# Performance work log

Measured on AMD Instinct MI355X. Metric: run time of the kernel, lower is better.

Reference implementation:

```python
import jax, jax.numpy as jnp
import numpy as np

ALPHA = 100.0
EPS = 1e-12  # matches torch F.normalize eps


def l2norm(v, axis):
    n = jnp.linalg.norm(v, axis=axis, keepdims=True)
    return v / jnp.maximum(n, EPS)


def setup_inputs() -> dict:
    key = jax.random.key(0)
    k1, k2 = jax.random.split(key)
    x = jax.random.normal(k1, (32, 512, 32, 32), dtype=jnp.float32)
    vocabs = jax.random.uniform(k2, (64, 512), dtype=jnp.float32)  # torch.rand init
    return {"x": x, "vocabs": vocabs}


def reference(x, vocabs):
    # x: [N, C, H, W]; vocabs: [K, C]
    N, C, H, W = x.shape
    K = vocabs.shape[0]
    x = l2norm(x, axis=1)                       # normalize descriptors over C
    xf = x.reshape(N, C, H * W)                 # [N, C, P]

    # 1x1 conv with weight = 2*alpha*vocabs, bias = -alpha*||vocabs||
    w = 2.0 * ALPHA * vocabs                    # [K, C]
    b = -ALPHA * jnp.linalg.norm(vocabs, axis=1)  # [K]
    logits = jnp.einsum('ncp,kc->nkp', xf, w) + b[None, :, None]
    a = jax.nn.softmax(logits, axis=1)          # soft assignment over K

    # Distributive rewrite of sum_p a[n,k,p]*(x[n,c,p] - vocabs[k,c])
    vlad = jnp.einsum('nkp,ncp->nkc', a, xf) - a.sum(-1)[:, :, None] * vocabs[None]
    vlad = l2norm(vlad, axis=2)                 # intra-normalization
    vlad = vlad.reshape(N, K * C)
    return l2norm(vlad, axis=1)
```

## Files before the change

kernel.cpp:

```cpp
#include <hip/hip_runtime.h>
#include <math.h>
#include <stdint.h>

#define ALPHA 100.0f
#define EPSN 1e-12f

typedef __attribute__((ext_vector_type(8))) short bf16x8;
typedef __attribute__((ext_vector_type(16))) float f32x16;
typedef __attribute__((ext_vector_type(4))) float f32x4;
typedef __attribute__((ext_vector_type(4))) unsigned int u32x4;

static __device__ __forceinline__ uint32_t f2bf(float f) {
    uint32_t u = __builtin_bit_cast(uint32_t, f);
    return (u + 0x7FFFu + ((u >> 16) & 1u)) >> 16;
}
static __device__ __forceinline__ float bfhi(uint32_t u) {
    return __builtin_bit_cast(float, u & 0xFFFF0000u);
}
static __device__ __forceinline__ uint32_t packbf(float a, float b) {
    return f2bf(a) | (f2bf(b) << 16);
}
static __device__ __forceinline__ void lds_barrier() {
    asm volatile("s_waitcnt lgkmcnt(0)\n\ts_barrier" ::: "memory");
}

__global__ __launch_bounds__(64) void prep_kernel(const float* __restrict__ v,
                                                  unsigned short* __restrict__ vh,
                                                  unsigned short* __restrict__ vl,
                                                  float* __restrict__ bias,
                                                  float* __restrict__ az) {
    int k = blockIdx.x, lane = threadIdx.x;
    az[k * 64 + lane] = 0.f;
    const float* row = v + k * 512;
    float ssq = 0.f;
#pragma unroll
    for (int i = 0; i < 8; ++i) {
        int c = lane + 64 * i;
        float f = row[c];
        ssq = fmaf(f, f, ssq);
        uint32_t hi = f2bf(f);
        uint32_t lo = f2bf(f - __builtin_bit_cast(float, hi << 16));
        vh[k * 512 + c] = (unsigned short)hi;
        vl[k * 512 + c] = (unsigned short)lo;
    }
#pragma unroll
    for (int off = 32; off > 0; off >>= 1) ssq += __shfl_xor(ssq, off, 64);
    if (lane == 0) bias[k] = -ALPHA * sqrtf(ssq);
}

__global__ __launch_bounds__(512) void fused_kernel(
    const float* __restrict__ x, const unsigned short* __restrict__ vh,
    const unsigned short* __restrict__ vl, const float* __restrict__ bias,
    float* __restrict__ pw, float* __restrict__ asum) {
    __shared__ uint32_t xsh[2][16 * 132];
    __shared__ uint32_t xsl[2][16 * 132];
    __shared__ float ssq_s[16][132];
    __shared__ float ssq_l[128];
    __shared__ float bias_l[64];
    __shared__ float xchm[4][2][32];
    __shared__ float xchs[4][2][32];
    __shared__ float a2f[64 * 132];
    __shared__ uint32_t xv[128 * 68];

    int tid = threadIdx.x, bx = blockIdx.x;
    int n = bx >> 3, pt = bx & 7, pblk = pt << 7;
    int l = tid & 63, w = tid >> 6;
    int kh = w & 1, ps = w >> 1;
    int h = l >> 5, cl = l & 31;
    int r = tid >> 5, q = tid & 31;

    if (tid < 64) bias_l[tid] = bias[tid];

    const float* xg = x + (size_t)n * 524288 + (size_t)(2 * r) * 1024 + pblk + 4 * q;
    const unsigned short* vhg = vh + (size_t)(32 * kh + cl) * 512 + 8 * h;
    const unsigned short* vlg = vl + (size_t)(32 * kh + cl) * 512 + 8 * h;

    f32x16 accA, accB;
#pragma unroll
    for (int i = 0; i < 16; ++i) { accA[i] = 0.f; accB[i] = 0.f; }
    f32x4 ssqv;
#pragma unroll
    for (int i = 0; i < 4; ++i) ssqv[i] = 0.f;

    float4 xa[3], xb[3];
    u32x4 vfh[3][2], vfl[3][2];

#define A_LOAD(slot, cc)                                                       \
    do {                                                                       \
        xa[slot] = *(const float4*)(xg + (size_t)(cc)*32768);                  \
        xb[slot] = *(const float4*)(xg + (size_t)(cc)*32768 + 1024);           \
        vfh[slot][0] = *(const u32x4*)(vhg + (cc)*32);                         \
        vfh[slot][1] = *(const u32x4*)(vhg + (cc)*32 + 16);                    \
        vfl[slot][0] = *(const u32x4*)(vlg + (cc)*32);                         \
        vfl[slot][1] = *(const u32x4*)(vlg + (cc)*32 + 16);                    \
    } while (0)
#define A_STAGE(buf, slot)                                                     \
    do {                                                                       \
        float fa[4] = {xa[slot].x, xa[slot].y, xa[slot].z, xa[slot].w};        \
        float fb[4] = {xb[slot].x, xb[slot].y, xb[slot].z, xb[slot].w};        \
        u32x4 hp, lp;                                                          \
        _Pragma("unroll") for (int i = 0; i < 4; ++i) {                        \
            uint32_t h0 = f2bf(fa[i]);                                         \
            uint32_t l0 = f2bf(fa[i] - bfhi(h0 << 16));                        \
            uint32_t h1 = f2bf(fb[i]);                                         \
            uint32_t l1 = f2bf(fb[i] - bfhi(h1 << 16));                        \
            hp[i] = h0 | (h1 << 16);                                           \
            lp[i] = l0 | (l1 << 16);                                           \
            ssqv[i] = fmaf(fa[i], fa[i], fmaf(fb[i], fb[i], ssqv[i]));         \
        }                                                                      \
        *(u32x4*)&xsh[buf][r * 132 + 4 * q] = hp;                              \
        *(u32x4*)&xsl[buf][r * 132 + 4 * q] = lp;                              \
    } while (0)
#define A_COMPUTE(buf, slot)                                                   \
    do {                                                                       \
        _Pragma("unroll") for (int s = 0; s < 2; ++s) {                        \
            int xb_ = (8 * s + 4 * h) * 132 + 32 * ps + cl;                    \
            u32x4 bhp, blp;                                                    \
            _Pragma("unroll") for (int q2 = 0; q2 < 4; ++q2) {                 \
                bhp[q2] = xsh[buf][xb_ + q2 * 132];                            \
                blp[q2] = xsl[buf][xb_ + q2 * 132];                            \
            }                                                                  \
            bf16x8 ah = __builtin_bit_cast(bf16x8, vfh[slot][s]);              \
            bf16x8 al = __builtin_bit_cast(bf16x8, vfl[slot][s]);              \
            bf16x8 xh_ = __builtin_bit_cast(bf16x8, bhp);                      \
            bf16x8 xl_ = __builtin_bit_cast(bf16x8, blp);                      \
            f32x16& accr = s ? accB : accA;                                    \
            accr = __builtin_amdgcn_mfma_f32_32x32x16_bf16(ah, xh_, accr, 0, 0, 0);\
            accr = __builtin_amdgcn_mfma_f32_32x32x16_bf16(ah, xl_, accr, 0, 0, 0);\
            accr = __builtin_amdgcn_mfma_f32_32x32x16_bf16(al, xh_, accr, 0, 0, 0);\
        }                                                                      \
    } while (0)

    A_LOAD(0, 0);
    A_LOAD(1, 1);
    A_LOAD(2, 2);
    A_STAGE(0, 0);
    lds_barrier();
#pragma unroll
    for (int cc = 0; cc < 16; ++cc) {
        if (cc < 15) A_STAGE((cc + 1) & 1, (cc + 1) % 3);
        A_COMPUTE(cc & 1, cc % 3);
        if (cc < 13) A_LOAD(cc % 3, cc + 3);
        lds_barrier();
    }
#undef A_LOAD
#undef A_STAGE
#undef A_COMPUTE

    *(f32x4*)&ssq_s[r][4 * q] = ssqv;
    __syncthreads();
    if (tid < 128) {
        float s = 0.f;
#pragma unroll
        for (int rr = 0; rr < 16; ++rr) s += ssq_s[rr][tid];
        ssq_l[tid] = s;
    }
    __syncthreads();
    float ssq = ssq_l[32 * ps + cl];
    float sinv = 1.0f / fmaxf(sqrtf(ssq), EPSN);
    float twoAs = 2.0f * ALPHA * sinv;
    float e[16];
    float m = -INFINITY;
#pragma unroll
    for (int rr = 0; rr < 16; ++rr) {
        int k = (rr & 3) + 8 * (rr >> 2) + 4 * h + 32 * kh;
        float lv = fmaf(twoAs, accA[rr] + accB[rr], bias_l[k]);
        e[rr] = lv;
        m = fmaxf(m, lv);
    }
    m = fmaxf(m, __shfl_xor(m, 32, 64));
    if (l < 32) xchm[ps][kh][l] = m;
    __syncthreads();
    m = fmaxf(m, xchm[ps][1 - kh][cl]);
    float ssum = 0.f;
#pragma unroll
    for (int rr = 0; rr < 16; ++rr) {
        e[rr] = expf(e[rr] - m);
        ssum += e[rr];
    }
    ssum += __shfl_xor(ssum, 32, 64);
    if (l < 32) xchs[ps][kh][l] = ssum;
    __syncthreads();
    ssum += xchs[ps][1 - kh][cl];
    float rs = 1.0f / ssum;
    float a2s = rs * sinv;
#pragma unroll
    for (int rr = 0; rr < 16; ++rr) {
        int k = (rr & 3) + 8 * (rr >> 2) + 4 * h + 32 * kh;
        a2f[k * 132 + 32 * ps + cl] = e[rr] * a2s;
        float red = e[rr] * rs;
#pragma unroll
        for (int off = 1; off <= 16; off <<= 1) red += __shfl_xor(red, off, 64);
        if (cl == 0) atomicAdd(&asum[n * 64 + k], red);
    }
    __syncthreads();

    f32x16 va0, va1, va2, va3;
#pragma unroll
    for (int i = 0; i < 16; ++i) { va0[i] = 0.f; va1[i] = 0.f; va2[i] = 0.f; va3[i] = 0.f; }

    int g = tid >> 2, u = tid & 3;
#pragma unroll
    for (int r2 = 0; r2 < 4; ++r2) {
        __syncthreads();
        {
            int c = (g >> 5) * 128 + r2 * 32 + (g & 31);
            const float* xs2 = x + (size_t)n * 524288 + (size_t)c * 1024 + pblk + 32 * u;
            float4 f0 = *(const float4*)(xs2);
            float4 f1 = *(const float4*)(xs2 + 4);
            float4 f2 = *(const float4*)(xs2 + 8);
            float4 f3 = *(const float4*)(xs2 + 12);
            float4 f4 = *(const float4*)(xs2 + 16);
            float4 f5 = *(const float4*)(xs2 + 20);
            float4 f6 = *(const float4*)(xs2 + 24);
            float4 f7 = *(const float4*)(xs2 + 28);
            u32x4 w0, w1, w2, w3;
            w0[0] = packbf(f0.x, f0.y); w0[1] = packbf(f0.z, f0.w);
            w0[2] = packbf(f1.x, f1.y); w0[3] = packbf(f1.z, f1.w);
            w1[0] = packbf(f2.x, f2.y); w1[1] = packbf(f2.z, f2.w);
            w1[2] = packbf(f3.x, f3.y); w1[3] = packbf(f3.z, f3.w);
            w2[0] = packbf(f4.x, f4.y); w2[1] = packbf(f4.z, f4.w);
            w2[2] = packbf(f5.x, f5.y); w2[3] = packbf(f5.z, f5.w);
            w3[0] = packbf(f6.x, f6.y); w3[1] = packbf(f6.z, f6.w);
            w3[2] = packbf(f7.x, f7.y); w3[3] = packbf(f7.z, f7.w);
            int xb0 = g * 68 + 16 * u;
            *(u32x4*)&xv[xb0] = w0;
            *(u32x4*)&xv[xb0 + 4] = w1;
            *(u32x4*)&xv[xb0 + 8] = w2;
            *(u32x4*)&xv[xb0 + 12] = w3;
        }
        __syncthreads();
        f32x16& vac = (r2 == 0) ? va0 : (r2 == 1) ? va1 : (r2 == 2) ? va2 : va3;
#pragma unroll
        for (int mm = 0; mm < 8; ++mm) {
            int ab = (32 * kh + cl) * 132 + 16 * mm + 8 * h;
            u32x4 af;
#pragma unroll
            for (int j = 0; j < 4; ++j)
                af[j] = packbf(a2f[ab + 2 * j], a2f[ab + 2 * j + 1]);
            int bb = (32 * ps + cl) * 68 + 8 * mm + 4 * h;
            u32x4 bf = *(const u32x4*)&xv[bb];
            vac = __builtin_amdgcn_mfma_f32_32x32x16_bf16(
                __builtin_bit_cast(bf16x8, af), __builtin_bit_cast(bf16x8, bf),
                vac, 0, 0, 0);
        }
    }
    float* pwb = pw + (((size_t)n * 8 + pt) * 64) * 512;
#pragma unroll
    for (int r2 = 0; r2 < 4; ++r2) {
        f32x16& vac = (r2 == 0) ? va0 : (r2 == 1) ? va1 : (r2 == 2) ? va2 : va3;
        int c = 128 * ps + 32 * r2 + cl;
#pragma unroll
        for (int rr = 0; rr < 16; ++rr) {
            int k = (rr & 3) + 8 * (rr >> 2) + 4 * h + 32 * kh;
            pwb[(size_t)k * 512 + c] = vac[rr];
        }
    }
}

__global__ __launch_bounds__(512) void combine_kernel(
    const float* __restrict__ pw, const float* __restrict__ asum,
    const float* __restrict__ vocabs, float* __restrict__ out) {
    __shared__ float lv[32768];
    __shared__ float knorm_l[64];
    __shared__ float sc[64];
    __shared__ float tots;

    int n = blockIdx.x, tid = threadIdx.x;
    int kq = tid >> 7, tc = tid & 127;
    const float* pwn = pw + (size_t)n * 262144;

#pragma unroll
    for (int ki = 0; ki < 16; ++ki) {
        int k = kq * 16 + ki;
        float a = asum[n * 64 + k];
        float4 vv = *(const float4*)(vocabs + (size_t)k * 512 + 4 * tc);
        float4 s = make_float4(0.f, 0.f, 0.f, 0.f);
#pragma unroll
        for (int pt = 0; pt < 8; ++pt) {
            float4 p4 = *(const float4*)(pwn + (size_t)pt * 32768 + (size_t)k * 512 + 4 * tc);
            s.x += p4.x; s.y += p4.y; s.z += p4.z; s.w += p4.w;
        }
        s.x = fmaf(-a, vv.x, s.x);
        s.y = fmaf(-a, vv.y, s.y);
        s.z = fmaf(-a, vv.z, s.z);
        s.w = fmaf(-a, vv.w, s.w);
        *(float4*)&lv[k * 512 + 4 * tc] = s;
    }
    __syncthreads();
    {
        int k2 = tid >> 3, j = tid & 7;
        float t2 = 0.f;
#pragma unroll
        for (int i = 0; i < 16; ++i) {
            float4 v4 = *(const float4*)&lv[k2 * 512 + j * 64 + 4 * i];
            t2 += v4.x * v4.x + v4.y * v4.y + v4.z * v4.z + v4.w * v4.w;
        }
        t2 += __shfl_xor(t2, 1, 64);
        t2 += __shfl_xor(t2, 2, 64);
        t2 += __shfl_xor(t2, 4, 64);
        if (j == 0) knorm_l[k2] = t2;
    }
    __syncthreads();
    if (tid < 64) {
        float nk = sqrtf(knorm_l[tid]);
        float inv = 1.0f / fmaxf(nk, EPSN);
        sc[tid] = inv;
        float t = nk * inv;
        float t2 = t * t;
#pragma unroll
        for (int off = 32; off > 0; off >>= 1) t2 += __shfl_xor(t2, off, 64);
        if (tid == 0) tots = t2;
    }
    __syncthreads();
    float invt = 1.0f / fmaxf(sqrtf(tots), EPSN);
    float* on = out + (size_t)n * 32768;
#pragma unroll
    for (int i = 0; i < 64; ++i) {
        int idx = tid + 512 * i;
        on[idx] = lv[idx] * sc[idx >> 9] * invt;
    }
}

extern "C" void kernel_launch(void* const* d_in, const int* in_sizes, int n_in,
                              void* d_out, int out_size, void* d_ws, size_t ws_size,
                              hipStream_t stream) {
    const float* x = (const float*)d_in[0];
    const float* vocabs = (const float*)d_in[1];
    float* out = (float*)d_out;
    char* ws = (char*)d_ws;
    unsigned short* vh = (unsigned short*)(ws);
    unsigned short* vl = (unsigned short*)(ws + 65536);
    float* bias  = (float*)(ws + 131072);
    float* asum  = (float*)(ws + 131328);
    float* pw    = (float*)(ws + 147712);

    prep_kernel<<<64, 64, 0, stream>>>(vocabs, vh, vl, bias, asum);
    fused_kernel<<<256, 512, 0, stream>>>(x, vh, vl, bias, pw, asum);
    combine_kernel<<<32, 512, 0, stream>>>(pw, asum, vocabs, out);
}
```

Before: 152.8 us.

## Stage full bf16 x tile in LDS once and reuse it for both GEMMs

Halves the pixel tile to 64 per block and doubles the grid to 512 blocks. Each block loads and splits its whole x tile (all 512 channels) into LDS up front, replacing the pipelined channel-chunk staging. The second GEMM (assignments times x) now reads the bf16-high copy of x from LDS instead of reloading x from global memory and repacking it. The first GEMM is split over channel halves across warps, with a cross-warp reduction through LDS. The partial-sum buffer doubles in size, so the combine kernel reads 16 partials per image instead of 8, which adds combine traffic and workspace.

```diff
diff --git a/kernel.cpp b/kernel.cpp
--- a/kernel.cpp
+++ b/kernel.cpp
@@ -16,12 +16,6 @@
 }
 static __device__ __forceinline__ float bfhi(uint32_t u) {
     return __builtin_bit_cast(float, u & 0xFFFF0000u);
-}
-static __device__ __forceinline__ uint32_t packbf(float a, float b) {
-    return f2bf(a) | (f2bf(b) << 16);
-}
-static __device__ __forceinline__ void lds_barrier() {
-    asm volatile("s_waitcnt lgkmcnt(0)\n\ts_barrier" ::: "memory");
 }
 
 __global__ __launch_bounds__(64) void prep_kernel(const float* __restrict__ v,
@@ -52,208 +46,194 @@
     const float* __restrict__ x, const unsigned short* __restrict__ vh,
     const unsigned short* __restrict__ vl, const float* __restrict__ bias,
     float* __restrict__ pw, float* __restrict__ asum) {
-    __shared__ uint32_t xsh[2][16 * 132];
-    __shared__ uint32_t xsl[2][16 * 132];
-    __shared__ float ssq_s[16][132];
-    __shared__ float ssq_l[128];
+    __shared__ uint32_t xallh[256 * 66];
+    __shared__ uint32_t xallo[256 * 64];
+    __shared__ float cmb[2][2][16][64];
+    __shared__ unsigned short a2b[64 * 72];
+    __shared__ float ssq_l[64];
     __shared__ float bias_l[64];
-    __shared__ float xchm[4][2][32];
-    __shared__ float xchs[4][2][32];
-    __shared__ float a2f[64 * 132];
-    __shared__ uint32_t xv[128 * 68];
+    __shared__ float xchm[2][2][32];
+    __shared__ float xchs[2][2][32];
 
     int tid = threadIdx.x, bx = blockIdx.x;
-    int n = bx >> 3, pt = bx & 7, pblk = pt << 7;
+    int n = bx >> 4, pt = bx & 15, pblk = pt << 6;
     int l = tid & 63, w = tid >> 6;
-    int kh = w & 1, ps = w >> 1;
     int h = l >> 5, cl = l & 31;
-    int r = tid >> 5, q = tid & 31;
-
-    if (tid < 64) bias_l[tid] = bias[tid];
-
-    const float* xg = x + (size_t)n * 524288 + (size_t)(2 * r) * 1024 + pblk + 4 * q;
-    const unsigned short* vhg = vh + (size_t)(32 * kh + cl) * 512 + 8 * h;
-    const unsigned short* vlg = vl + (size_t)(32 * kh + cl) * 512 + 8 * h;
+
+    if (tid < 64) {
+        ssq_l[tid] = 0.f;
+        bias_l[tid] = bias[tid];
+    }
+
+    int r0 = tid >> 4, q = tid & 15;
+    const float* xgs = x + (size_t)n * 524288 + (size_t)(2 * r0) * 1024 + pblk + 4 * q;
+    float4 va_[8], vb_[8];
+#pragma unroll
+    for (int i = 0; i < 8; ++i) {
+        va_[i] = *(const float4*)(xgs + (size_t)i * 65536);
+        vb_[i] = *(const float4*)(xgs + (size_t)i * 65536 + 1024);
+    }
+    __syncthreads();
+    f32x4 sq;
+#pragma unroll
+    for (int j = 0; j < 4; ++j) sq[j] = 0.f;
+#pragma unroll
+    for (int i = 0; i < 8; ++i) {
+        int R = r0 + 32 * i;
+        float fa[4] = {va_[i].x, va_[i].y, va_[i].z, va_[i].w};
+        float fb[4] = {vb_[i].x, vb_[i].y, vb_[i].z, vb_[i].w};
+        uint32_t hp[4];
+        u32x4 lp;
+#pragma unroll
+        for (int j = 0; j < 4; ++j) {
+            uint32_t h0 = f2bf(fa[j]);
+            uint32_t l0 = f2bf(fa[j] - bfhi(h0 << 16));
+            uint32_t h1 = f2bf(fb[j]);
+            uint32_t l1 = f2bf(fb[j] - bfhi(h1 << 16));
+            hp[j] = h0 | (h1 << 16);
+            lp[j] = l0 | (l1 << 16);
+            sq[j] = fmaf(fa[j], fa[j], fmaf(fb[j], fb[j], sq[j]));
+        }
+        *(uint2*)&xallh[R * 66 + 4 * q] = make_uint2(hp[0], hp[1]);
+        *(uint2*)&xallh[R * 66 + 4 * q + 2] = make_uint2(hp[2], hp[3]);
+        *(u32x4*)&xallo[R * 64 + 4 * q] = lp;
+    }
+#pragma unroll
+    for (int j = 0; j < 4; ++j) atomicAdd(&ssq_l[4 * q + j], sq[j]);
+    __syncthreads();
+
+    int kh = w & 1, pj = (w >> 1) & 1, ch = w >> 2;
+    const unsigned short* vhg = vh + (size_t)(32 * kh + cl) * 512 + 256 * ch + 8 * h;
+    const unsigned short* vlg = vl + (size_t)(32 * kh + cl) * 512 + 256 * ch + 8 * h;
 
     f32x16 accA, accB;
 #pragma unroll
     for (int i = 0; i < 16; ++i) { accA[i] = 0.f; accB[i] = 0.f; }
-    f32x4 ssqv;
-#pragma unroll
-    for (int i = 0; i < 4; ++i) ssqv[i] = 0.f;
-
-    float4 xa[3], xb[3];
-    u32x4 vfh[3][2], vfl[3][2];
-
-#define A_LOAD(slot, cc)                                                       \
-    do {                                                                       \
-        xa[slot] = *(const float4*)(xg + (size_t)(cc)*32768);                  \
-        xb[slot] = *(const float4*)(xg + (size_t)(cc)*32768 + 1024);           \
-        vfh[slot][0] = *(const u32x4*)(vhg + (cc)*32);                         \
-        vfh[slot][1] = *(const u32x4*)(vhg + (cc)*32 + 16);                    \
-        vfl[slot][0] = *(const u32x4*)(vlg + (cc)*32);                         \
-        vfl[slot][1] = *(const u32x4*)(vlg + (cc)*32 + 16);                    \
-    } while (0)
-#define A_STAGE(buf, slot)                                                     \
-    do {                                                                       \
-        float fa[4] = {xa[slot].x, xa[slot].y, xa[slot].z, xa[slot].w};        \
-        float fb[4] = {xb[slot].x, xb[slot].y, xb[slot].z, xb[slot].w};        \
-        u32x4 hp, lp;                                                          \
-        _Pragma("unroll") for (int i = 0; i < 4; ++i) {                        \
-            uint32_t h0 = f2bf(fa[i]);                                         \
-            uint32_t l0 = f2bf(fa[i] - bfhi(h0 << 16));                        \
-            uint32_t h1 = f2bf(fb[i]);                                         \
-            uint32_t l1 = f2bf(fb[i] - bfhi(h1 << 16));                        \
-            hp[i] = h0 | (h1 << 16);                                           \
-            lp[i] = l0 | (l1 << 16);                                           \
-            ssqv[i] = fmaf(fa[i], fa[i], fmaf(fb[i], fb[i], ssqv[i]));         \
-        }                                                                      \
-        *(u32x4*)&xsh[buf][r * 132 + 4 * q] = hp;                              \
-        *(u32x4*)&xsl[buf][r * 132 + 4 * q] = lp;                              \
-    } while (0)
-#define A_COMPUTE(buf, slot)                                                   \
-    do {                                                                       \
-        _Pragma("unroll") for (int s = 0; s < 2; ++s) {                        \
-            int xb_ = (8 * s + 4 * h) * 132 + 32 * ps + cl;                    \
-            u32x4 bhp, blp;                                                    \
-            _Pragma("unroll") for (int q2 = 0; q2 < 4; ++q2) {                 \
-                bhp[q2] = xsh[buf][xb_ + q2 * 132];                            \
-                blp[q2] = xsl[buf][xb_ + q2 * 132];                            \
-            }                                                                  \
-            bf16x8 ah = __builtin_bit_cast(bf16x8, vfh[slot][s]);              \
-            bf16x8 al = __builtin_bit_cast(bf16x8, vfl[slot][s]);              \
-            bf16x8 xh_ = __builtin_bit_cast(bf16x8, bhp);                      \
-            bf16x8 xl_ = __builtin_bit_cast(bf16x8, blp);                      \
-            f32x16& accr = s ? accB : accA;                                    \
-            accr = __builtin_amdgcn_mfma_f32_32x32x16_bf16(ah, xh_, accr, 0, 0, 0);\
-            accr = __builtin_amdgcn_mfma_f32_32x32x16_bf16(ah, xl_, accr, 0, 0, 0);\
-            accr = __builtin_amdgcn_mfma_f32_32x32x16_bf16(al, xh_, accr, 0, 0, 0);\
-        }                                                                      \
-    } while (0)
-
-    A_LOAD(0, 0);
-    A_LOAD(1, 1);
-    A_LOAD(2, 2);
-    A_STAGE(0, 0);
-    lds_barrier();
-#pragma unroll
-    for (int cc = 0; cc < 16; ++cc) {
-        if (cc < 15) A_STAGE((cc + 1) & 1, (cc + 1) % 3);
-        A_COMPUTE(cc & 1, cc % 3);
-        if (cc < 13) A_LOAD(cc % 3, cc + 3);
-        lds_barrier();
-    }
-#undef A_LOAD
-#undef A_STAGE
-#undef A_COMPUTE
-
-    *(f32x4*)&ssq_s[r][4 * q] = ssqv;
-    __syncthreads();
-    if (tid < 128) {
-        float s = 0.f;
-#pragma unroll
-        for (int rr = 0; rr < 16; ++rr) s += ssq_s[rr][tid];
-        ssq_l[tid] = s;
-    }
-    __syncthreads();
-    float ssq = ssq_l[32 * ps + cl];
-    float sinv = 1.0f / fmaxf(sqrtf(ssq), EPSN);
-    float twoAs = 2.0f * ALPHA * sinv;
-    float e[16];
-    float m = -INFINITY;
-#pragma unroll
-    for (int rr = 0; rr < 16; ++rr) {
-        int k = (rr & 3) + 8 * (rr >> 2) + 4 * h + 32 * kh;
-        float lv = fmaf(twoAs, accA[rr] + accB[rr], bias_l[k]);
-        e[rr] = lv;
-        m = fmaxf(m, lv);
-    }
-    m = fmaxf(m, __shfl_xor(m, 32, 64));
-    if (l < 32) xchm[ps][kh][l] = m;
-    __syncthreads();
-    m = fmaxf(m, xchm[ps][1 - kh][cl]);
-    float ssum = 0.f;
-#pragma unroll
-    for (int rr = 0; rr < 16; ++rr) {
-        e[rr] = expf(e[rr] - m);
-        ssum += e[rr];
-    }
-    ssum += __shfl_xor(ssum, 32, 64);
-    if (l < 32) xchs[ps][kh][l] = ssum;
-    __syncthreads();
-    ssum += xchs[ps][1 - kh][cl];
-    float rs = 1.0f / ssum;
-    float a2s = rs * sinv;
-#pragma unroll
-    for (int rr = 0; rr < 16; ++rr) {
-        int k = (rr & 3) + 8 * (rr >> 2) + 4 * h + 32 * kh;
-        a2f[k * 132 + 32 * ps + cl] = e[rr] * a2s;
-        float red = e[rr] * rs;
-#pragma unroll
-        for (int off = 1; off <= 16; off <<= 1) red += __shfl_xor(red, off, 64);
-        if (cl == 0) atomicAdd(&asum[n * 64 + k], red);
-    }
-    __syncthreads();
-
-    f32x16 va0, va1, va2, va3;
-#pragma unroll
-    for (int i = 0; i < 16; ++i) { va0[i] = 0.f; va1[i] = 0.f; va2[i] = 0.f; va3[i] = 0.f; }
-
-    int g = tid >> 2, u = tid & 3;
-#pragma unroll
-    for (int r2 = 0; r2 < 4; ++r2) {
-        __syncthreads();
-        {
-            int c = (g >> 5) * 128 + r2 * 32 + (g & 31);
-            const float* xs2 = x + (size_t)n * 524288 + (size_t)c * 1024 + pblk + 32 * u;
-            float4 f0 = *(const float4*)(xs2);
-            float4 f1 = *(const float4*)(xs2 + 4);
-            float4 f2 = *(const float4*)(xs2 + 8);
-            float4 f3 = *(const float4*)(xs2 + 12);
-            float4 f4 = *(const float4*)(xs2 + 16);
-            float4 f5 = *(const float4*)(xs2 + 20);
-            float4 f6 = *(const float4*)(xs2 + 24);
-            float4 f7 = *(const float4*)(xs2 + 28);
-            u32x4 w0, w1, w2, w3;
-            w0[0] = packbf(f0.x, f0.y); w0[1] = packbf(f0.z, f0.w);
-            w0[2] = packbf(f1.x, f1.y); w0[3] = packbf(f1.z, f1.w);
-            w1[0] = packbf(f2.x, f2.y); w1[1] = packbf(f2.z, f2.w);
-            w1[2] = packbf(f3.x, f3.y); w1[3] = packbf(f3.z, f3.w);
-            w2[0] = packbf(f4.x, f4.y); w2[1] = packbf(f4.z, f4.w);
-            w2[2] = packbf(f5.x, f5.y); w2[3] = packbf(f5.z, f5.w);
-            w3[0] = packbf(f6.x, f6.y); w3[1] = packbf(f6.z, f6.w);
-            w3[2] = packbf(f7.x, f7.y); w3[3] = packbf(f7.z, f7.w);
-            int xb0 = g * 68 + 16 * u;
-            *(u32x4*)&xv[xb0] = w0;
-            *(u32x4*)&xv[xb0 + 4] = w1;
-            *(u32x4*)&xv[xb0 + 8] = w2;
-            *(u32x4*)&xv[xb0 + 12] = w3;
-        }
-        __syncthreads();
-        f32x16& vac = (r2 == 0) ? va0 : (r2 == 1) ? va1 : (r2 == 2) ? va2 : va3;
-#pragma unroll
-        for (int mm = 0; mm < 8; ++mm) {
-            int ab = (32 * kh + cl) * 132 + 16 * mm + 8 * h;
-            u32x4 af;
-#pragma unroll
-            for (int j = 0; j < 4; ++j)
-                af[j] = packbf(a2f[ab + 2 * j], a2f[ab + 2 * j + 1]);
-            int bb = (32 * ps + cl) * 68 + 8 * mm + 4 * h;
-            u32x4 bf = *(const u32x4*)&xv[bb];
-            vac = __builtin_amdgcn_mfma_f32_32x32x16_bf16(
-                __builtin_bit_cast(bf16x8, af), __builtin_bit_cast(bf16x8, bf),
-                vac, 0, 0, 0);
-        }
-    }
-    float* pwb = pw + (((size_t)n * 8 + pt) * 64) * 512;
-#pragma unroll
-    for (int r2 = 0; r2 < 4; ++r2) {
-        f32x16& vac = (r2 == 0) ? va0 : (r2 == 1) ? va1 : (r2 == 2) ? va2 : va3;
-        int c = 128 * ps + 32 * r2 + cl;
+
+    u32x4 pvh[2][2], pvl[2][2];
+    pvh[0][0] = *(const u32x4*)(vhg);
+    pvh[0][1] = *(const u32x4*)(vhg + 16);
+    pvl[0][0] = *(const u32x4*)(vlg);
+    pvl[0][1] = *(const u32x4*)(vlg + 16);
+#pragma unroll
+    for (int cc = 0; cc < 8; ++cc) {
+        int cur = cc & 1;
+        if (cc < 7) {
+            pvh[cur ^ 1][0] = *(const u32x4*)(vhg + 32 * (cc + 1));
+            pvh[cur ^ 1][1] = *(const u32x4*)(vhg + 32 * (cc + 1) + 16);
+            pvl[cur ^ 1][0] = *(const u32x4*)(vlg + 32 * (cc + 1));
+            pvl[cur ^ 1][1] = *(const u32x4*)(vlg + 32 * (cc + 1) + 16);
+        }
+#pragma unroll
+        for (int s = 0; s < 2; ++s) {
+            u32x4 bhp, blp;
+#pragma unroll
+            for (int q2 = 0; q2 < 4; ++q2) {
+                int R = 128 * ch + 16 * cc + 8 * s + 4 * h + q2;
+                bhp[q2] = xallh[R * 66 + 32 * pj + cl];
+                blp[q2] = xallo[R * 64 + 32 * pj + cl];
+            }
+            bf16x8 ah = __builtin_bit_cast(bf16x8, pvh[cur][s]);
+            bf16x8 al = __builtin_bit_cast(bf16x8, pvl[cur][s]);
+            bf16x8 xh = __builtin_bit_cast(bf16x8, bhp);
+            bf16x8 xl = __builtin_bit_cast(bf16x8, blp);
+            f32x16& accr = s ? accB : accA;
+            accr = __builtin_amdgcn_mfma_f32_32x32x16_bf16(ah, xh, accr, 0, 0, 0);
+            accr = __builtin_amdgcn_mfma_f32_32x32x16_bf16(ah, xl, accr, 0, 0, 0);
+            accr = __builtin_amdgcn_mfma_f32_32x32x16_bf16(al, xh, accr, 0, 0, 0);
+        }
+    }
+
+    if (ch == 1) {
+#pragma unroll
+        for (int rr = 0; rr < 16; ++rr) cmb[kh][pj][rr][l] = accA[rr] + accB[rr];
+    }
+    __syncthreads();
+    float e[16], m = -INFINITY, ssum = 0.f, sinv = 0.f;
+    if (ch == 0) {
+        float ssq = ssq_l[32 * pj + cl];
+        sinv = 1.0f / fmaxf(sqrtf(ssq), EPSN);
+        float twoAs = 2.0f * ALPHA * sinv;
 #pragma unroll
         for (int rr = 0; rr < 16; ++rr) {
             int k = (rr & 3) + 8 * (rr >> 2) + 4 * h + 32 * kh;
-            pwb[(size_t)k * 512 + c] = vac[rr];
+            float dv = accA[rr] + accB[rr] + cmb[kh][pj][rr][l];
+            float lv = fmaf(twoAs, dv, bias_l[k]);
+            e[rr] = lv;
+            m = fmaxf(m, lv);
+        }
+        m = fmaxf(m, __shfl_xor(m, 32, 64));
+        if (l < 32) xchm[pj][kh][l] = m;
+    }
+    __syncthreads();
+    if (ch == 0) {
+        m = fmaxf(m, xchm[pj][1 - kh][cl]);
+#pragma unroll
+        for (int rr = 0; rr < 16; ++rr) {
+            e[rr] = expf(e[rr] - m);
+            ssum += e[rr];
+        }
+        ssum += __shfl_xor(ssum, 32, 64);
+        if (l < 32) xchs[pj][kh][l] = ssum;
+    }
+    __syncthreads();
+    if (ch == 0) {
+        ssum += xchs[pj][1 - kh][cl];
+        float rs = 1.0f / ssum;
+        float a2s = rs * sinv;
+#pragma unroll
+        for (int rr = 0; rr < 16; ++rr) {
+            int k = (rr & 3) + 8 * (rr >> 2) + 4 * h + 32 * kh;
+            a2b[k * 72 + 32 * pj + cl] = (unsigned short)f2bf(e[rr] * a2s);
+            float red = e[rr] * rs;
+#pragma unroll
+            for (int off = 1; off <= 16; off <<= 1) red += __shfl_xor(red, off, 64);
+            if (cl == 0) atomicAdd(&asum[n * 64 + k], red);
+        }
+    }
+    __syncthreads();
+
+    int cq = w >> 1;
+    const uint32_t* a2w = (const uint32_t*)a2b;
+    u32x4 af[4];
+#pragma unroll
+    for (int kc = 0; kc < 4; ++kc)
+        af[kc] = *(const u32x4*)&a2w[(32 * kh + cl) * 36 + 8 * kc + 4 * h];
+
+    f32x16 va[4];
+#pragma unroll
+    for (int j = 0; j < 4; ++j)
+#pragma unroll
+        for (int i = 0; i < 16; ++i) va[j][i] = 0.f;
+
+#pragma unroll
+    for (int j = 0; j < 4; ++j) {
+        int c = 128 * cq + 32 * j + cl;
+        int cp = c >> 1;
+        uint32_t odd = (uint32_t)(c & 1);
+#pragma unroll
+        for (int kc = 0; kc < 4; ++kc) {
+            u32x4 bfv;
+#pragma unroll
+            for (int jj = 0; jj < 4; ++jj) {
+                uint2 wp = *(const uint2*)&xallh[cp * 66 + 16 * kc + 8 * h + 2 * jj];
+                uint32_t lo = (wp.x & 0xFFFFu) | (wp.y << 16);
+                uint32_t hi = (wp.x >> 16) | (wp.y & 0xFFFF0000u);
+                bfv[jj] = odd ? hi : lo;
+            }
+            va[j] = __builtin_amdgcn_mfma_f32_32x32x16_bf16(
+                __builtin_bit_cast(bf16x8, af[kc]), __builtin_bit_cast(bf16x8, bfv),
+                va[j], 0, 0, 0);
+        }
+    }
+    float* pwb = pw + ((size_t)(n * 16 + pt) * 64) * 512;
+#pragma unroll
+    for (int j = 0; j < 4; ++j) {
+        int c = 128 * cq + 32 * j + cl;
+#pragma unroll
+        for (int rr = 0; rr < 16; ++rr) {
+            int k = (rr & 3) + 8 * (rr >> 2) + 4 * h + 32 * kh;
+            pwb[(size_t)k * 512 + c] = va[j][rr];
         }
     }
 }
@@ -268,7 +248,7 @@
 
     int n = blockIdx.x, tid = threadIdx.x;
     int kq = tid >> 7, tc = tid & 127;
-    const float* pwn = pw + (size_t)n * 262144;
+    const float* pwn = pw + (size_t)n * 524288;
 
 #pragma unroll
     for (int ki = 0; ki < 16; ++ki) {
@@ -277,7 +257,7 @@
         float4 vv = *(const float4*)(vocabs + (size_t)k * 512 + 4 * tc);
         float4 s = make_float4(0.f, 0.f, 0.f, 0.f);
 #pragma unroll
-        for (int pt = 0; pt < 8; ++pt) {
+        for (int pt = 0; pt < 16; ++pt) {
             float4 p4 = *(const float4*)(pwn + (size_t)pt * 32768 + (size_t)k * 512 + 4 * tc);
             s.x += p4.x; s.y += p4.y; s.z += p4.z; s.w += p4.w;
         }
@@ -336,6 +316,6 @@
     float* pw    = (float*)(ws + 147712);
 
     prep_kernel<<<64, 64, 0, stream>>>(vocabs, vh, vl, bias, asum);
-    fused_kernel<<<256, 512, 0, stream>>>(x, vh, vl, bias, pw, asum);
+    fused_kernel<<<512, 512, 0, stream>>>(x, vh, vl, bias, pw, asum);
     combine_kernel<<<32, 512, 0, stream>>>(pw, asum, vocabs, out);
 }
```

After: 163.9 us. 1.07x slower.
